# Optimization experiments

Measured on AMD Instinct MI355X. Metric: run time of the kernel, lower is better.

Reference implementation:

```python
import jax, jax.numpy as jnp
import numpy as np

DIM = 256
B = 8
SPATIAL = 4096
TB = B * SPATIAL
DT_REF = 1.0
MAX_GROWTH = 0.3


def _dft_matrix(n):
    idx = jnp.arange(n, dtype=jnp.float32)
    phase = -2.0 * jnp.pi * idx[None, :] * idx[:, None] / n
    return ((jnp.cos(phase) + 1j * jnp.sin(phase)) / jnp.sqrt(jnp.float32(n))).astype(jnp.complex64)


def setup_inputs() -> dict:
    key = jax.random.key(0)
    ks = jax.random.split(key, 24)
    D = DIM
    inp = {
        'h_re': jax.random.normal(ks[0], (TB, 1, D), jnp.float32),
        'h_im': jax.random.normal(ks[1], (TB, 1, D), jnp.float32),
        'x_re': jax.random.normal(ks[2], (TB, D), jnp.float32),
        'x_im': jax.random.normal(ks[3], (TB, D), jnp.float32),
        'xg_re': jax.random.normal(ks[4], (B, D), jnp.float32),
        'xg_im': jax.random.normal(ks[5], (B, D), jnp.float32),
        'flux_re': jax.random.normal(ks[6], (B, D), jnp.float32),
        'flux_im': jax.random.normal(ks[7], (B, D), jnp.float32),
        # ComplexSVDTransform params (U init ~ identity + noise, like trained state)
        'U_re': jnp.eye(D, dtype=jnp.float32) + 0.02 * jax.random.normal(ks[8], (D, D), jnp.float32),
        'U_im': 0.02 * jax.random.normal(ks[9], (D, D), jnp.float32),
        'dft_w': jnp.float32(0.2),
        # GlobalFluxTracker params
        'decay_re': 0.1 * jax.random.normal(ks[10], (D,), jnp.float32),
        'decay_im': 0.1 * jax.random.normal(ks[11], (D,), jnp.float32),
        'Wm': jnp.eye(2 * D, dtype=jnp.float32) + 0.02 * jax.random.normal(ks[12], (2 * D, 2 * D), jnp.float32),
        'bm': jnp.zeros((2 * D,), jnp.float32),
        'Wp': 0.04 * jax.random.normal(ks[13], (2 * D, 2 * D), jnp.float32),
        'bp': jnp.zeros((2 * D,), jnp.float32),
        'Wg': 0.05 * jax.random.normal(ks[14], (D, 2 * D), jnp.float32),
        'bg': jnp.zeros((D,), jnp.float32),
        # lambda eigenvalues
        'lam_re': 0.01 * jax.random.normal(ks[15], (D,), jnp.float32),
        'lam_im': 0.1 * jax.random.normal(ks[16], (D,), jnp.float32),
        'dt': 1,
    }
    return inp


def reference(h_re, h_im, x_re, x_im, xg_re, xg_im, flux_re, flux_im,
              U_re, U_im, dft_w, decay_re, decay_im, Wm, bm, Wp, bp, Wg, bg,
              lam_re, lam_im, dt):
    D = U_re.shape[0]
    # --- ComplexSVDTransform.encode ---
    U = (U_re + 1j * U_im).astype(jnp.complex64)
    dft = _dft_matrix(D)
    w = jax.nn.sigmoid(dft_w)
    x = (x_re + 1j * x_im)  # [TB, D] complex
    x_tilde = (1.0 - w) * (x @ U) + w * (x @ dft)
    x_tilde = x_tilde[:, None, :]  # [TB, 1, D] (ndim==2 -> unsqueeze(1))

    # --- GlobalFluxTracker.forward_step ---
    fdecay = jax.nn.sigmoid(decay_re) + 1j * decay_im  # [D]
    xg_cat = jnp.concatenate([xg_re, xg_im], axis=-1)  # [B, 2D]
    x_in = xg_cat @ Wm.T + bm
    update = x_in[:, :D] + 1j * x_in[:, D:]
    flux_state = flux_re + 1j * flux_im
    flux_next = flux_state * fdecay + update  # [B, D]
    s_cat = jnp.concatenate([flux_next.real, flux_next.imag], axis=-1)  # [B, 2D]
    proj = s_cat @ Wp.T + bp
    source = proj[:, :D] + 1j * proj[:, D:]  # [B, D]
    gate = jnp.clip(jax.nn.sigmoid(s_cat @ Wg.T + bg), 0.01, 0.99)  # [B, D]

    # --- transition operators (exp/expm1 discretization of lam*dt) ---
    lam_re_b = jnp.clip(lam_re, -MAX_GROWTH, MAX_GROWTH)
    lam = lam_re_b + 1j * lam_im
    dt_ratio = jnp.float32(dt) / DT_REF
    exp_arg = lam * dt_ratio
    op_decay = jnp.exp(exp_arg)  # [D]
    lam_safe = lam + 1e-8 * jnp.sign(lam_re_b + 1e-12)
    op_forcing = (op_decay - 1.0) / lam_safe  # expm1(exp_arg)/lam_safe

    # --- gated forcing and state update ---
    tb = x_tilde.shape[0]
    b = source.shape[0]
    spatial = tb // b
    src_e = jnp.broadcast_to(source[:, None, None, :], (b, spatial, 1, D)).reshape(tb, 1, D)
    gate_e = jnp.broadcast_to(gate[:, None, None, :].astype(jnp.complex64), (b, spatial, 1, D)).reshape(tb, 1, D)
    forcing_term = x_tilde * gate_e + src_e * (1.0 - gate_e)
    h_prev = h_re + 1j * h_im  # [TB, 1, D]
    h_next = h_prev * op_decay + forcing_term * op_forcing
    return (h_next, flux_next)
```

## Files before the change

### kernel.cpp

```cpp
#include <hip/hip_runtime.h>
#include <math.h>

#define D 256
#define TBROWS 32768
#define BATCH 8

typedef __attribute__((ext_vector_type(4)))  float f32x4;
typedef __attribute__((ext_vector_type(16))) float f32x16;
typedef __attribute__((ext_vector_type(8)))  short short8v;
typedef __attribute__((ext_vector_type(4)))  short short4v;

#define WS_OD   0
#define WS_C1   512
#define WS_C0   4608
#define WS_BHI  8704
#define WS_BLO  139776

__device__ __forceinline__ float sigmoidf_(float x){ return 1.0f/(1.0f+expf(-x)); }
__device__ __forceinline__ unsigned short f2bf(float f){
  unsigned int u = __float_as_uint(f);
  unsigned int r = (u + 0x7FFFu + ((u>>16)&1u)) >> 16;
  return (unsigned short)r;
}
__device__ __forceinline__ float bf2f(unsigned short h){
  return __uint_as_float(((unsigned int)h)<<16);
}

__global__ void prep_batch_kernel(const float* __restrict__ xg_re, const float* __restrict__ xg_im,
                                  const float* __restrict__ flux_re, const float* __restrict__ flux_im,
                                  const float* __restrict__ Wm, const float* __restrict__ bm,
                                  const float* __restrict__ decay_re, const float* __restrict__ decay_im,
                                  const float* __restrict__ Wp, const float* __restrict__ bp,
                                  const float* __restrict__ Wg, const float* __restrict__ bg,
                                  const float* __restrict__ lam_re, const float* __restrict__ lam_im,
                                  const int* __restrict__ dt_p,
                                  float* __restrict__ ws, float* __restrict__ out_flux, int cplx){
  __shared__ float vin[512];
  __shared__ float mid[768];
  const int b = blockIdx.x, j = threadIdx.x;
  if (j < 512) vin[j] = (j < D) ? xg_re[b*D + j] : xg_im[b*D + (j - D)];
  __syncthreads();
  if (j < 512){
    const float4* row4 = (const float4*)(Wm + j*512);
    const float4* x4p  = (const float4*)vin;
    float acc = 0.f;
    #pragma unroll 8
    for (int k = 0; k < 128; ++k){
      float4 w4 = row4[k]; float4 x4 = x4p[k];
      acc += w4.x*x4.x + w4.y*x4.y + w4.z*x4.z + w4.w*x4.w;
    }
    mid[j] = acc + bm[j];
  }
  __syncthreads();
  if (j < D){
    float ur = mid[j], ui = mid[D + j];
    float fdr = sigmoidf_(decay_re[j]);
    float fdi = decay_im[j];
    float fr = flux_re[b*D + j], fi = flux_im[b*D + j];
    float nr = fr*fdr - fi*fdi + ur;
    float ni = fr*fdi + fi*fdr + ui;
    vin[j]     = nr;
    vin[D + j] = ni;
    if (cplx){ out_flux[(b*D + j)*2] = nr; out_flux[(b*D + j)*2 + 1] = ni; }
    else     { out_flux[b*D + j] = nr; }
  }
  __syncthreads();
  {
    const float* rowp = (j < 512) ? (Wp + j*512) : (Wg + (j - 512)*512);
    float bias = (j < 512) ? bp[j] : bg[j - 512];
    const float4* row4 = (const float4*)rowp;
    const float4* x4p  = (const float4*)vin;
    float acc = 0.f;
    #pragma unroll 8
    for (int k = 0; k < 128; ++k){
      float4 w4 = row4[k]; float4 x4 = x4p[k];
      acc += w4.x*x4.x + w4.y*x4.y + w4.z*x4.z + w4.w*x4.w;
    }
    mid[j] = acc + bias;
  }
  __syncthreads();
  if (j < D){
    float sr = mid[j], si = mid[D + j];
    float g = sigmoidf_(mid[512 + j]);
    g = fminf(fmaxf(g, 0.01f), 0.99f);
    float lrb = fminf(fmaxf(lam_re[j], -0.3f), 0.3f);
    float li  = lam_im[j];
    float dtr = (float)dt_p[0];
    float er  = expf(lrb * dtr);
    float ang = li * dtr;
    float odr = er * cosf(ang), odi = er * sinf(ang);
    float sarg = lrb + 1e-12f;
    float sgn = (sarg > 0.f) ? 1.f : ((sarg < 0.f) ? -1.f : 0.f);
    float lrs = lrb + 1e-8f * sgn;
    float nr = odr - 1.f, ni = odi;
    float den = lrs*lrs + li*li;
    float ofr = (nr*lrs + ni*li) / den;
    float ofi = (ni*lrs - nr*li) / den;
    ws[WS_C1 + (b*D + j)*2]     = g * ofr;
    ws[WS_C1 + (b*D + j)*2 + 1] = g * ofi;
    float s1r = sr*(1.f - g), s1i = si*(1.f - g);
    ws[WS_C0 + (b*D + j)*2]     = s1r*ofr - s1i*ofi;
    ws[WS_C0 + (b*D + j)*2 + 1] = s1r*ofi + s1i*ofr;
    if (b == 0){
      ws[WS_OD + j*2]     = odr;
      ws[WS_OD + j*2 + 1] = odi;
    }
  }
}

__global__ void prep_B_kernel(const float* __restrict__ U_re, const float* __restrict__ U_im,
                              const float* __restrict__ dft_w, float* __restrict__ ws){
  const int kp = blockIdx.x;
  const int jj = threadIdx.x;
  const int k  = kp & 255, half = kp >> 8;
  const int j  = jj >> 1,  part = jj & 1;
  float w = sigmoidf_(dft_w[0]);
  const float c = -6.283185307179586f;
  float t1 = c * (float)j;
  float ph = (t1 * (float)k) / 256.0f;
  float dre = cosf(ph) * 0.0625f;
  float dim = sinf(ph) * 0.0625f;
  float mr = (1.f - w)*U_re[k*D + j] + w*dre;
  float mi = (1.f - w)*U_im[k*D + j] + w*dim;
  float V = part ? (half ? mr : mi) : (half ? -mi : mr);
  unsigned short hi = f2bf(V);
  unsigned short lo = f2bf(V - bf2f(hi));
  int s = kp >> 4, rb = kp & 15;
  int hi5 = rb >> 3, j8 = rb & 7;
  int ct = jj >> 5, lane = hi5*32 + (jj & 31);
  size_t off = ((size_t)(s*16 + ct)*64 + lane)*8 + j8;
  ((unsigned short*)(ws + WS_BHI))[off] = hi;
  ((unsigned short*)(ws + WS_BLO))[off] = lo;
}

__global__ __launch_bounds__(1024) void main_mfma_kernel(
    const float* __restrict__ x_re, const float* __restrict__ x_im,
    const float* __restrict__ h_re, const float* __restrict__ h_im,
    const float* __restrict__ ws, float* __restrict__ out, int cplx){
  __shared__ short Ahi[4096];
  __shared__ short Alo[4096];
  const int tid  = threadIdx.x;
  const int lane = tid & 63;
  const int ct   = tid >> 6;
  const int row0 = blockIdx.x * 64;
  const int b    = row0 >> 12;
  const unsigned short* Bh0 = (const unsigned short*)(ws + WS_BHI);
  const unsigned short* Bl0 = (const unsigned short*)(ws + WS_BLO);

  f32x16 acc0 = {}; f32x16 acc1 = {};

  const int srow = tid >> 4, sseg = tid & 15;
  const int ssl  = sseg >> 2;
  const int sk16 = (sseg & 3) * 4;
  const int soff = ((((ssl*2) + (srow>>5))*64) + (sk16>>3)*32 + (srow&31))*8 + (sk16&7);

  for (int c = 0; c < 8; ++c){
    __syncthreads();
    {
      const float* src = (c < 4) ? x_re : x_im;
      const int koff = (c & 3)*64;
      f32x4 v = *(const f32x4*)(src + (size_t)(row0 + srow)*256 + koff + sseg*4);
      short4v hv, lv;
      #pragma unroll
      for (int q = 0; q < 4; ++q){
        float f = v[q];
        unsigned short hb = f2bf(f);
        hv[q] = (short)hb;
        lv[q] = (short)f2bf(f - bf2f(hb));
      }
      *(short4v*)&Ahi[soff] = hv;
      *(short4v*)&Alo[soff] = lv;
    }
    __syncthreads();
    #pragma unroll
    for (int sl = 0; sl < 4; ++sl){
      short8v ah0 = *(const short8v*)&Ahi[((sl*2+0)*64 + lane)*8];
      short8v al0 = *(const short8v*)&Alo[((sl*2+0)*64 + lane)*8];
      short8v ah1 = *(const short8v*)&Ahi[((sl*2+1)*64 + lane)*8];
      short8v al1 = *(const short8v*)&Alo[((sl*2+1)*64 + lane)*8];
      const size_t boff = ((size_t)((c*4+sl)*16 + ct)*64 + lane)*8;
      short8v bh = *(const short8v*)(Bh0 + boff);
      short8v bl = *(const short8v*)(Bl0 + boff);
      acc0 = __builtin_amdgcn_mfma_f32_32x32x16_bf16(ah0, bh, acc0, 0,0,0);
      acc1 = __builtin_amdgcn_mfma_f32_32x32x16_bf16(ah1, bh, acc1, 0,0,0);
      acc0 = __builtin_amdgcn_mfma_f32_32x32x16_bf16(al0, bh, acc0, 0,0,0);
      acc1 = __builtin_amdgcn_mfma_f32_32x32x16_bf16(al1, bh, acc1, 0,0,0);
      acc0 = __builtin_amdgcn_mfma_f32_32x32x16_bf16(ah0, bl, acc0, 0,0,0);
      acc1 = __builtin_amdgcn_mfma_f32_32x32x16_bf16(ah1, bl, acc1, 0,0,0);
    }
  }

  const int j = ct*16 + ((lane & 31) >> 1);
  const int part = lane & 1;
  const float odr = ws[WS_OD + j*2],           odi = ws[WS_OD + j*2 + 1];
  const float c1r = ws[WS_C1 + (b*D + j)*2],   c1i = ws[WS_C1 + (b*D + j)*2 + 1];
  const float c0r = ws[WS_C0 + (b*D + j)*2],   c0i = ws[WS_C0 + (b*D + j)*2 + 1];
  #pragma unroll
  for (int rt = 0; rt < 2; ++rt){
    #pragma unroll
    for (int r = 0; r < 16; ++r){
      float val = (rt == 0) ? acc0[r] : acc1[r];
      float other = __shfl_xor(val, 1);
      float xr = part ? other : val;
      float xi = part ? val   : other;
      int row = row0 + rt*32 + 4*(lane>>5) + (r & 3) + 8*(r >> 2);
      float hr = h_re[(size_t)row*256 + j];
      float hi = h_im[(size_t)row*256 + j];
      float ore = hr*odr - hi*odi + xr*c1r - xi*c1i + c0r;
      float oim = hr*odi + hi*odr + xr*c1i + xi*c1r + c0i;
      if (cplx){
        out[((size_t)row*256 + j)*2 + part] = part ? oim : ore;
      } else if (!part){
        out[(size_t)row*256 + j] = ore;
      }
    }
  }
}

extern "C" void kernel_launch(void* const* d_in, const int* in_sizes, int n_in,
                              void* d_out, int out_size, void* d_ws, size_t ws_size,
                              hipStream_t stream){
  const float* h_re    = (const float*)d_in[0];
  const float* h_im    = (const float*)d_in[1];
  const float* x_re    = (const float*)d_in[2];
  const float* x_im    = (const float*)d_in[3];
  const float* xg_re   = (const float*)d_in[4];
  const float* xg_im   = (const float*)d_in[5];
  const float* flux_re = (const float*)d_in[6];
  const float* flux_im = (const float*)d_in[7];
  const float* U_re    = (const float*)d_in[8];
  const float* U_im    = (const float*)d_in[9];
  const float* dft_w   = (const float*)d_in[10];
  const float* decay_re= (const float*)d_in[11];
  const float* decay_im= (const float*)d_in[12];
  const float* Wm      = (const float*)d_in[13];
  const float* bm      = (const float*)d_in[14];
  const float* Wp      = (const float*)d_in[15];
  const float* bp      = (const float*)d_in[16];
  const float* Wg      = (const float*)d_in[17];
  const float* bg      = (const float*)d_in[18];
  const float* lam_re  = (const float*)d_in[19];
  const float* lam_im  = (const float*)d_in[20];
  const int*   dt      = (const int*)d_in[21];
  float* ws  = (float*)d_ws;
  float* out = (float*)d_out;

  const int cplx = (out_size >= 2*TBROWS*D) ? 1 : 0;
  float* out_flux = out + (size_t)TBROWS*D*(cplx ? 2 : 1);

  prep_batch_kernel<<<BATCH, 768, 0, stream>>>(xg_re, xg_im, flux_re, flux_im, Wm, bm,
                                               decay_re, decay_im, Wp, bp, Wg, bg,
                                               lam_re, lam_im, dt, ws, out_flux, cplx);
  prep_B_kernel<<<512, 512, 0, stream>>>(U_re, U_im, dft_w, ws);
  main_mfma_kernel<<<TBROWS/64, 1024, 0, stream>>>(x_re, x_im, h_re, h_im, ws, out, cplx);
}
```

Baseline: 339.4 us.

## Split main GEMM into 64-column blocks with double-buffered LDS prefetch

The main MFMA kernel moves from 1024-thread blocks covering all 256 output columns to 256-thread blocks that each compute a 64x64 output tile. This quadruples the grid. The K loop becomes 16 chunks of 32 with a double-buffered LDS stage: the next chunk's x values are prefetched into registers during the MFMAs, then converted and written to the alternate buffer, leaving one barrier per iteration instead of two. A block-index swizzle groups the four column blocks of a row tile so the repeated x reads can hit in cache. The trade-off is that each x row is now loaded and split into hi/lo bf16 four times, once per column block.

```diff
diff --git a/kernel.cpp b/kernel.cpp
--- a/kernel.cpp
+++ b/kernel.cpp
@@ -8,7 +8,6 @@
 typedef __attribute__((ext_vector_type(4)))  float f32x4;
 typedef __attribute__((ext_vector_type(16))) float f32x16;
 typedef __attribute__((ext_vector_type(8)))  short short8v;
-typedef __attribute__((ext_vector_type(4)))  short short4v;
 
 #define WS_OD   0
 #define WS_C1   512
@@ -133,54 +132,71 @@
   ((unsigned short*)(ws + WS_BLO))[off] = lo;
 }
 
-__global__ __launch_bounds__(1024) void main_mfma_kernel(
+__global__ __launch_bounds__(256, 4) void main_mfma_kernel(
     const float* __restrict__ x_re, const float* __restrict__ x_im,
     const float* __restrict__ h_re, const float* __restrict__ h_im,
     const float* __restrict__ ws, float* __restrict__ out, int cplx){
-  __shared__ short Ahi[4096];
-  __shared__ short Alo[4096];
+  __shared__ short Ah[2][2048];
+  __shared__ short Al[2][2048];
   const int tid  = threadIdx.x;
   const int lane = tid & 63;
-  const int ct   = tid >> 6;
-  const int row0 = blockIdx.x * 64;
+  const int wv   = tid >> 6;
+  const int bid  = blockIdx.x;
+  const int swz  = (bid & 7)*256 + (bid >> 3);
+  const int cb   = swz & 3;
+  const int row0 = (swz >> 2) * 64;
   const int b    = row0 >> 12;
+  const int CT   = cb*4 + wv;
   const unsigned short* Bh0 = (const unsigned short*)(ws + WS_BHI);
   const unsigned short* Bl0 = (const unsigned short*)(ws + WS_BLO);
 
   f32x16 acc0 = {}; f32x16 acc1 = {};
 
-  const int srow = tid >> 4, sseg = tid & 15;
-  const int ssl  = sseg >> 2;
-  const int sk16 = (sseg & 3) * 4;
-  const int soff = ((((ssl*2) + (srow>>5))*64) + (sk16>>3)*32 + (srow&31))*8 + (sk16&7);
-
-  for (int c = 0; c < 8; ++c){
+  const int srow = tid >> 2;
+  const int kb   = (tid & 3) * 8;
+  const int soff = (((kb>>4)*2 + (srow>>5))*64 + ((kb>>3)&1)*32 + (srow&31))*8;
+
+  f32x4 p0, p1;
+  auto loadx = [&](int c){
+    const float* src = (c < 8) ? x_re : x_im;
+    const float* base = src + (size_t)(row0 + srow)*256 + (c & 7)*32 + kb;
+    p0 = *(const f32x4*)base;
+    p1 = *(const f32x4*)(base + 4);
+  };
+  auto cvt_write = [&](int buf){
+    short8v hv, lv;
+    #pragma unroll
+    for (int q = 0; q < 4; ++q){
+      float f = p0[q];
+      unsigned short hb = f2bf(f);
+      hv[q] = (short)hb; lv[q] = (short)f2bf(f - bf2f(hb));
+    }
+    #pragma unroll
+    for (int q = 0; q < 4; ++q){
+      float f = p1[q];
+      unsigned short hb = f2bf(f);
+      hv[4+q] = (short)hb; lv[4+q] = (short)f2bf(f - bf2f(hb));
+    }
+    *(short8v*)&Ah[buf][soff] = hv;
+    *(short8v*)&Al[buf][soff] = lv;
+  };
+
+  loadx(0);
+  cvt_write(0);
+  int cur = 0;
+  for (int c = 0; c < 16; ++c){
     __syncthreads();
-    {
-      const float* src = (c < 4) ? x_re : x_im;
-      const int koff = (c & 3)*64;
-      f32x4 v = *(const f32x4*)(src + (size_t)(row0 + srow)*256 + koff + sseg*4);
-      short4v hv, lv;
-      #pragma unroll
-      for (int q = 0; q < 4; ++q){
-        float f = v[q];
-        unsigned short hb = f2bf(f);
-        hv[q] = (short)hb;
-        lv[q] = (short)f2bf(f - bf2f(hb));
-      }
-      *(short4v*)&Ahi[soff] = hv;
-      *(short4v*)&Alo[soff] = lv;
-    }
-    __syncthreads();
-    #pragma unroll
-    for (int sl = 0; sl < 4; ++sl){
-      short8v ah0 = *(const short8v*)&Ahi[((sl*2+0)*64 + lane)*8];
-      short8v al0 = *(const short8v*)&Alo[((sl*2+0)*64 + lane)*8];
-      short8v ah1 = *(const short8v*)&Ahi[((sl*2+1)*64 + lane)*8];
-      short8v al1 = *(const short8v*)&Alo[((sl*2+1)*64 + lane)*8];
-      const size_t boff = ((size_t)((c*4+sl)*16 + ct)*64 + lane)*8;
+    if (c < 15) loadx(c + 1);
+    #pragma unroll
+    for (int sl = 0; sl < 2; ++sl){
+      const int g = sl*2;
+      const size_t boff = ((size_t)((c*2 + sl)*16 + CT)*64 + lane)*8;
       short8v bh = *(const short8v*)(Bh0 + boff);
       short8v bl = *(const short8v*)(Bl0 + boff);
+      short8v ah0 = *(const short8v*)&Ah[cur][((g+0)*64 + lane)*8];
+      short8v al0 = *(const short8v*)&Al[cur][((g+0)*64 + lane)*8];
+      short8v ah1 = *(const short8v*)&Ah[cur][((g+1)*64 + lane)*8];
+      short8v al1 = *(const short8v*)&Al[cur][((g+1)*64 + lane)*8];
       acc0 = __builtin_amdgcn_mfma_f32_32x32x16_bf16(ah0, bh, acc0, 0,0,0);
       acc1 = __builtin_amdgcn_mfma_f32_32x32x16_bf16(ah1, bh, acc1, 0,0,0);
       acc0 = __builtin_amdgcn_mfma_f32_32x32x16_bf16(al0, bh, acc0, 0,0,0);
@@ -188,9 +204,11 @@
       acc0 = __builtin_amdgcn_mfma_f32_32x32x16_bf16(ah0, bl, acc0, 0,0,0);
       acc1 = __builtin_amdgcn_mfma_f32_32x32x16_bf16(ah1, bl, acc1, 0,0,0);
     }
-  }
-
-  const int j = ct*16 + ((lane & 31) >> 1);
+    if (c < 15) cvt_write(cur ^ 1);
+    cur ^= 1;
+  }
+
+  const int j = cb*64 + wv*16 + ((lane & 31) >> 1);
   const int part = lane & 1;
   const float odr = ws[WS_OD + j*2],           odi = ws[WS_OD + j*2 + 1];
   const float c1r = ws[WS_C1 + (b*D + j)*2],   c1i = ws[WS_C1 + (b*D + j)*2 + 1];
@@ -252,5 +270,5 @@
                                                decay_re, decay_im, Wp, bp, Wg, bg,
                                                lam_re, lam_im, dt, ws, out_flux, cplx);
   prep_B_kernel<<<512, 512, 0, stream>>>(U_re, U_im, dft_w, ws);
-  main_mfma_kernel<<<TBROWS/64, 1024, 0, stream>>>(x_re, x_im, h_re, h_im, ws, out, cplx);
-}
+  main_mfma_kernel<<<2048, 256, 0, stream>>>(x_re, x_im, h_re, h_im, ws, out, cplx);
+}
```

Measured after the change: 354.0 us. 4.3% more time.
